# Performance work log

Hardware: AMD Instinct MI355X
Metric: run time of the kernel (lower is better)

Reference implementation:

```python
import jax, jax.numpy as jnp
import numpy as np

SEQ, BATCH, IN_DIM, HID = 2048, 32, 512, 512


def setup_inputs() -> dict:
    key = jax.random.key(0)
    ks = jax.random.split(key, 5)
    scale_ih = 1.0 / np.sqrt(HID)
    return {
        "x": jax.random.normal(ks[0], (SEQ, BATCH, IN_DIM), dtype=jnp.float32),
        "h0": jnp.zeros((BATCH, HID), dtype=jnp.float32),
        "c0": jnp.zeros((BATCH, HID), dtype=jnp.float32),
        "W_ih": jax.random.uniform(ks[1], (4 * HID, IN_DIM), dtype=jnp.float32, minval=-scale_ih, maxval=scale_ih),
        "W_hh": jax.random.uniform(ks[2], (4 * HID, HID), dtype=jnp.float32, minval=-scale_ih, maxval=scale_ih),
        "b_ih": jax.random.uniform(ks[3], (4 * HID,), dtype=jnp.float32, minval=-scale_ih, maxval=scale_ih),
        "b_hh": jax.random.uniform(ks[4], (4 * HID,), dtype=jnp.float32, minval=-scale_ih, maxval=scale_ih),
    }


def reference(x, h0, c0, W_ih, W_hh, b_ih, b_hh):
    # torch.nn.LSTMCell gate order: input, forget, cell(g), output
    b = b_ih + b_hh
    # Precompute input projections for all timesteps: [S, B, 4H]
    x_proj = jnp.einsum("sbi,gi->sbg", x, W_ih) + b

    def step(carry, xp_t):
        h, c = carry
        gates = xp_t + h @ W_hh.T  # [B, 4H]
        i, f, g, o = jnp.split(gates, 4, axis=-1)
        i = jax.nn.sigmoid(i)
        f = jax.nn.sigmoid(f)
        g = jnp.tanh(g)
        o = jax.nn.sigmoid(o)
        c_new = f * c + i * g
        h_new = o * jnp.tanh(c_new)
        return (h_new, c_new), h_new

    (h_T, c_T), hs = jax.lax.scan(step, (h0, c0), x_proj)
    return hs, h_T, c_T
```

## Files before the change

### kernel.cpp

```cpp
#include <hip/hip_runtime.h>
#include <math.h>

#define SEQ    2048
#define BATCH  32
#define IN_DIM 512
#define HID    512
#define GATES  (4*HID)

typedef __attribute__((ext_vector_type(4))) float f32x4;
typedef __attribute__((ext_vector_type(2))) float f32x2;

__device__ inline float fsigmoid(float x) {
    return 1.f / (1.f + __expf(-x));
}
__device__ inline float ftanh(float x) {
    return 1.f - 2.f / (1.f + __expf(2.f * x));
}

__global__ __launch_bounds__(256) void xproj_kernel(
    const float* __restrict__ x,
    const float* __restrict__ Wih,
    const float* __restrict__ bih,
    const float* __restrict__ bhh,
    float* __restrict__ xp,
    int M)
{
    __shared__ float As[16][132];
    __shared__ float Bs[16][132];
    const int tid = threadIdx.x;
    const int nb = blockIdx.x & 15;
    const int mb = blockIdx.x >> 4;
    const int m0 = mb * 128, n0 = nb * 128;
    const int tx = tid & 15, ty = tid >> 4;

    float acc[8][8];
#pragma unroll
    for (int i = 0; i < 8; ++i)
#pragma unroll
        for (int j = 0; j < 8; ++j) acc[i][j] = 0.f;

    for (int kc = 0; kc < 512; kc += 16) {
#pragma unroll
        for (int h = 0; h < 2; ++h) {
            int f4 = tid + 256 * h;
            int r = f4 >> 2, u = f4 & 3;
            float4 va = *(const float4*)(x + (size_t)(m0 + r) * 512 + kc + 4 * u);
            As[4*u+0][r] = va.x; As[4*u+1][r] = va.y;
            As[4*u+2][r] = va.z; As[4*u+3][r] = va.w;
            float4 vb = *(const float4*)(Wih + (size_t)(n0 + r) * 512 + kc + 4 * u);
            Bs[4*u+0][r] = vb.x; Bs[4*u+1][r] = vb.y;
            Bs[4*u+2][r] = vb.z; Bs[4*u+3][r] = vb.w;
        }
        __syncthreads();
#pragma unroll
        for (int kk = 0; kk < 16; ++kk) {
            float4 a0 = *(const float4*)&As[kk][tx * 8];
            float4 a1 = *(const float4*)&As[kk][tx * 8 + 4];
            float4 b0 = *(const float4*)&Bs[kk][ty * 8];
            float4 b1 = *(const float4*)&Bs[kk][ty * 8 + 4];
            float av[8] = {a0.x,a0.y,a0.z,a0.w,a1.x,a1.y,a1.z,a1.w};
            float bv[8] = {b0.x,b0.y,b0.z,b0.w,b1.x,b1.y,b1.z,b1.w};
#pragma unroll
            for (int i = 0; i < 8; ++i)
#pragma unroll
                for (int j = 0; j < 8; ++j) acc[i][j] += av[i] * bv[j];
        }
        __syncthreads();
    }

    float bias[8];
#pragma unroll
    for (int j = 0; j < 8; ++j) {
        int n = n0 + ty * 8 + j;
        bias[j] = bih[n] + bhh[n];
    }
#pragma unroll
    for (int i = 0; i < 8; ++i) {
        size_t base = (size_t)(m0 + tx * 8 + i) * GATES + n0 + ty * 8;
        float4 v0 = make_float4(acc[i][0]+bias[0], acc[i][1]+bias[1],
                                acc[i][2]+bias[2], acc[i][3]+bias[3]);
        float4 v1 = make_float4(acc[i][4]+bias[4], acc[i][5]+bias[5],
                                acc[i][6]+bias[6], acc[i][7]+bias[7]);
        *(float4*)(xp + base)     = v0;
        *(float4*)(xp + base + 4) = v1;
    }
}

__global__ __launch_bounds__(256, 1)
__attribute__((amdgpu_waves_per_eu(1, 1)))
void lstm_coop(
    const float* __restrict__ Whh,
    const float* __restrict__ xp,
    float* __restrict__ hx,
    float* __restrict__ cbuf,
    float* __restrict__ out_hs,
    int t0, int nsteps)
{
    const int w    = blockIdx.x;
    const int g    = w >> 5;
    const int sl   = w & 31;
    const int tid  = threadIdx.x;
    const int hw   = tid >> 6;
    const int lane = tid & 63;
    const int rr   = (lane >> 4) & 3;
    const int kg   = lane & 15;

    __shared__ f32x4 h4[2][512];

    f32x4 wv[32];
#pragma unroll
    for (int gi = 0; gi < 4; ++gi) {
        const float* wr = Whh + (size_t)(512*gi + 16*sl + 4*hw + rr) * 512 + 32*kg;
#pragma unroll
        for (int q = 0; q < 8; ++q) {
            asm volatile("global_load_dwordx4 %0, %1, off"
                         : "=v"(wv[gi*8+q]) : "v"(wr + 4*q));
        }
    }
    asm volatile("s_waitcnt vmcnt(0)" ::: "memory");

    const bool is_tail = ((lane & 12) == 0);
    const int  jb      = lane & 3;
    const int  hid_gl  = 16*sl + 4*hw + rr;
    const int  b_gl    = 4*g + jb;
    const int  slot_p  = 16*(hid_gl & 31) + (hid_gl >> 5);

    float c_reg = 0.f;
    if (is_tail) c_reg = cbuf[(size_t)b_gl * HID + hid_gl];

    for (int t = t0; t < t0 + nsteps; ++t) {
        const int p = t & 1;
        const int xrow = 512*(kg >> 2) + 16*sl + 4*hw + rr;
        const int xb   = 4*g + (kg & 3);
        float xpv = xp[(size_t)(t - t0) * (BATCH * GATES)
                       + (size_t)xb * GATES + xrow];

        const float* rb = hx + ((size_t)p * 8 + g) * 4096;
        const float* p0 = rb + 8 * tid;
        const float* p1 = rb + 8 * tid + 2048;
        const unsigned tu = __float_as_uint((float)t);
        f32x2 a0, a1, a2, a3, b0, b1, b2, b3;
        while (true) {
            asm volatile(
                "global_load_dwordx2 %0, %8, off sc0 sc1\n\t"
                "global_load_dwordx2 %1, %8, off offset:8 sc0 sc1\n\t"
                "global_load_dwordx2 %2, %8, off offset:16 sc0 sc1\n\t"
                "global_load_dwordx2 %3, %8, off offset:24 sc0 sc1\n\t"
                "global_load_dwordx2 %4, %9, off sc0 sc1\n\t"
                "global_load_dwordx2 %5, %9, off offset:8 sc0 sc1\n\t"
                "global_load_dwordx2 %6, %9, off offset:16 sc0 sc1\n\t"
                "global_load_dwordx2 %7, %9, off offset:24 sc0 sc1\n\t"
                "s_waitcnt vmcnt(0)"
                : "=&v"(a0), "=&v"(a1), "=&v"(a2), "=&v"(a3),
                  "=&v"(b0), "=&v"(b1), "=&v"(b2), "=&v"(b3)
                : "v"(p0), "v"(p1)
                : "memory");
            if (__float_as_uint(a0[1]) == tu && __float_as_uint(a1[1]) == tu &&
                __float_as_uint(a2[1]) == tu && __float_as_uint(a3[1]) == tu &&
                __float_as_uint(b0[1]) == tu && __float_as_uint(b1[1]) == tu &&
                __float_as_uint(b2[1]) == tu && __float_as_uint(b3[1]) == tu)
                break;
            __builtin_amdgcn_s_sleep(1);
        }
        {
            f32x4 v0 = {a0[0], a1[0], a2[0], a3[0]};
            f32x4 v1 = {b0[0], b1[0], b2[0], b3[0]};
            h4[p][tid]       = v0;
            h4[p][tid + 256] = v1;
        }
        __syncthreads();

        float acc[16];
#pragma unroll
        for (int m = 0; m < 16; ++m) acc[m] = 0.f;
#pragma unroll
        for (int s = 0; s < 32; ++s) {
            f32x4 hv = h4[p][16*s + kg];
#pragma unroll
            for (int gi = 0; gi < 4; ++gi) {
                float wt = wv[gi*8 + (s >> 2)][s & 3];
                acc[4*gi+0] += wt * hv[0];
                acc[4*gi+1] += wt * hv[1];
                acc[4*gi+2] += wt * hv[2];
                acc[4*gi+3] += wt * hv[3];
            }
        }

        {
            int sel = (kg >> 3) & 1;
#pragma unroll
            for (int m = 0; m < 8; ++m) {
                float mine = sel ? acc[m+8] : acc[m];
                float send = sel ? acc[m]   : acc[m+8];
                acc[m] = mine + __shfl_xor(send, 8, 64);
            }
        }
        {
            int sel = (kg >> 2) & 1;
#pragma unroll
            for (int m = 0; m < 4; ++m) {
                float mine = sel ? acc[m+4] : acc[m];
                float send = sel ? acc[m]   : acc[m+4];
                acc[m] = mine + __shfl_xor(send, 4, 64);
            }
        }
        {
            int sel = (kg >> 1) & 1;
#pragma unroll
            for (int m = 0; m < 2; ++m) {
                float mine = sel ? acc[m+2] : acc[m];
                float send = sel ? acc[m]   : acc[m+2];
                acc[m] = mine + __shfl_xor(send, 2, 64);
            }
        }
        {
            int sel = kg & 1;
            float mine = sel ? acc[1] : acc[0];
            float send = sel ? acc[0] : acc[1];
            acc[0] = mine + __shfl_xor(send, 1, 64);
        }

        float gval = acc[0] + xpv;
        float fv2 = __shfl(gval, (lane & 48) + 4  + jb);
        float gv2 = __shfl(gval, (lane & 48) + 8  + jb);
        float ov2 = __shfl(gval, (lane & 48) + 12 + jb);

        if (is_tail) {
            float iv = fsigmoid(gval);
            float fv = fsigmoid(fv2);
            float gv = ftanh(gv2);
            float ov = fsigmoid(ov2);
            float cn = fv * c_reg + iv * gv;
            float hn = ov * ftanh(cn);
            c_reg = cn;
            f32x2 pkt;
            pkt[0] = hn;
            pkt[1] = (float)(t + 1);
            float* wp = hx + ((size_t)((t + 1) & 1) * 8 + g) * 4096
                        + 8 * slot_p + 2 * jb;
            asm volatile("global_store_dwordx2 %0, %1, off sc0 sc1"
                         :: "v"(wp), "v"(pkt) : "memory");
            out_hs[(size_t)t * (BATCH * HID) + (size_t)b_gl * HID + hid_gl] = hn;
        }
    }

    if (is_tail) cbuf[(size_t)b_gl * HID + hid_gl] = c_reg;
}

__global__ void init_kernel(const float* __restrict__ h0,
                            const float* __restrict__ c0,
                            float* __restrict__ hx,
                            float* __restrict__ cbuf)
{
    int idx = blockIdx.x * 256 + threadIdx.x;
    if (idx < 16384) {
        int g = idx >> 11, G = idx & 2047;
        int slot = G >> 2, c = G & 3;
        int k = 32 * (slot & 15) + (slot >> 4);
        int b = 4 * g + c;
        hx[(size_t)g * 4096 + 2*G]     = h0[(size_t)b * HID + k];
        hx[(size_t)g * 4096 + 2*G + 1] = 0.0f;
        hx[(size_t)32768 + (size_t)g * 4096 + 2*G]     = 0.0f;
        hx[(size_t)32768 + (size_t)g * 4096 + 2*G + 1] = __uint_as_float(0xFFFFFFFFu);
        cbuf[idx] = c0[idx];
    }
}

__global__ void tail_kernel(const float* __restrict__ hx,
                            const float* __restrict__ cbuf,
                            float* __restrict__ out)
{
    int idx = blockIdx.x * 256 + threadIdx.x;
    if (idx < BATCH * HID) {
        int b = idx >> 9, k = idx & 511;
        int g = b >> 2, c = b & 3;
        int slot = 16 * (k & 31) + (k >> 5);
        int G = 4 * slot + c;
        out[(size_t)SEQ * BATCH * HID + idx] = hx[(size_t)g * 4096 + 2*G];
        out[(size_t)SEQ * BATCH * HID + BATCH * HID + idx] = cbuf[idx];
    }
}

extern "C" void kernel_launch(void* const* d_in, const int* in_sizes, int n_in,
                              void* d_out, int out_size, void* d_ws, size_t ws_size,
                              hipStream_t stream)
{
    const float* x   = (const float*)d_in[0];
    const float* h0  = (const float*)d_in[1];
    const float* c0  = (const float*)d_in[2];
    const float* Wih = (const float*)d_in[3];
    const float* Whh = (const float*)d_in[4];
    const float* bih = (const float*)d_in[5];
    const float* bhh = (const float*)d_in[6];
    float* out = (float*)d_out;

    float* hx   = (float*)d_ws;
    float* cbuf = hx + 65536;
    float* xp   = cbuf + 16384;
    size_t used_floats = 65536 + 16384;
    size_t avail = (ws_size / 4 > used_floats) ? (ws_size / 4 - used_floats) : 0;
    int chunk = (int)(avail / (size_t)(BATCH * GATES));
    if (chunk > SEQ) chunk = SEQ;
    chunk &= ~3;
    if (chunk < 4) chunk = 4;

    hipLaunchKernelGGL(init_kernel, dim3(64), dim3(256), 0, stream,
                       h0, c0, hx, cbuf);

    for (int t0 = 0; t0 < SEQ; t0 += chunk) {
        int n = SEQ - t0; if (n > chunk) n = chunk;
        int M = n * BATCH;
        hipLaunchKernelGGL(xproj_kernel, dim3(16 * (M / 128)), dim3(256), 0, stream,
                           x + (size_t)t0 * BATCH * IN_DIM, Wih, bih, bhh, xp, M);

        const float* xp_c = xp;
        int t0_arg = t0, n_arg = n;
        void* args[] = { (void*)&Whh, (void*)&xp_c, (void*)&hx, (void*)&cbuf,
                         (void*)&out, (void*)&t0_arg, (void*)&n_arg };
        hipLaunchCooperativeKernel((void*)lstm_coop, dim3(256), dim3(256),
                                   args, 0, stream);
    }

    hipLaunchKernelGGL(tail_kernel, dim3(64), dim3(256), 0, stream,
                       hx, cbuf, out);
}
```

Measured before the change: 9.368 ms.

## Add fast-path spin with sc1-only loads and prefetch next xproj value

The h-exchange polling loop first spins without sleep using loads scoped only by sc1, which may hit a nearer cache level. After 200 failed polls it falls back to the original sc0 sc1 loads with s_sleep. The producer now writes each packet twice, once with sc1 and once with sc0 sc1, so both cache scopes see the new value. The input-projection load for the next step is issued after polling so its latency overlaps the matvec, at the cost of an extra store per step and possible stale-read retries.

```diff
diff --git a/kernel.cpp b/kernel.cpp
--- a/kernel.cpp
+++ b/kernel.cpp
@@ -128,40 +128,72 @@
     float c_reg = 0.f;
     if (is_tail) c_reg = cbuf[(size_t)b_gl * HID + hid_gl];
 
+    const int xrow = 512*(kg >> 2) + 16*sl + 4*hw + rr;
+    const int xb   = 4*g + (kg & 3);
+    const size_t xoff = (size_t)xb * GATES + xrow;
+
+    float xpv_cur = xp[xoff];
+    bool  fast = true;
+
     for (int t = t0; t < t0 + nsteps; ++t) {
         const int p = t & 1;
-        const int xrow = 512*(kg >> 2) + 16*sl + 4*hw + rr;
-        const int xb   = 4*g + (kg & 3);
-        float xpv = xp[(size_t)(t - t0) * (BATCH * GATES)
-                       + (size_t)xb * GATES + xrow];
 
         const float* rb = hx + ((size_t)p * 8 + g) * 4096;
         const float* p0 = rb + 8 * tid;
         const float* p1 = rb + 8 * tid + 2048;
         const unsigned tu = __float_as_uint((float)t);
         f32x2 a0, a1, a2, a3, b0, b1, b2, b3;
-        while (true) {
-            asm volatile(
-                "global_load_dwordx2 %0, %8, off sc0 sc1\n\t"
-                "global_load_dwordx2 %1, %8, off offset:8 sc0 sc1\n\t"
-                "global_load_dwordx2 %2, %8, off offset:16 sc0 sc1\n\t"
-                "global_load_dwordx2 %3, %8, off offset:24 sc0 sc1\n\t"
-                "global_load_dwordx2 %4, %9, off sc0 sc1\n\t"
-                "global_load_dwordx2 %5, %9, off offset:8 sc0 sc1\n\t"
-                "global_load_dwordx2 %6, %9, off offset:16 sc0 sc1\n\t"
-                "global_load_dwordx2 %7, %9, off offset:24 sc0 sc1\n\t"
-                "s_waitcnt vmcnt(0)"
-                : "=&v"(a0), "=&v"(a1), "=&v"(a2), "=&v"(a3),
-                  "=&v"(b0), "=&v"(b1), "=&v"(b2), "=&v"(b3)
-                : "v"(p0), "v"(p1)
-                : "memory");
-            if (__float_as_uint(a0[1]) == tu && __float_as_uint(a1[1]) == tu &&
-                __float_as_uint(a2[1]) == tu && __float_as_uint(a3[1]) == tu &&
-                __float_as_uint(b0[1]) == tu && __float_as_uint(b1[1]) == tu &&
-                __float_as_uint(b2[1]) == tu && __float_as_uint(b3[1]) == tu)
-                break;
-            __builtin_amdgcn_s_sleep(1);
-        }
+        {
+            int it = 0;
+            while (true) {
+                if (fast) {
+                    asm volatile(
+                        "global_load_dwordx2 %0, %8, off sc1\n\t"
+                        "global_load_dwordx2 %1, %8, off offset:8 sc1\n\t"
+                        "global_load_dwordx2 %2, %8, off offset:16 sc1\n\t"
+                        "global_load_dwordx2 %3, %8, off offset:24 sc1\n\t"
+                        "global_load_dwordx2 %4, %9, off sc1\n\t"
+                        "global_load_dwordx2 %5, %9, off offset:8 sc1\n\t"
+                        "global_load_dwordx2 %6, %9, off offset:16 sc1\n\t"
+                        "global_load_dwordx2 %7, %9, off offset:24 sc1\n\t"
+                        "s_waitcnt vmcnt(0)"
+                        : "=&v"(a0), "=&v"(a1), "=&v"(a2), "=&v"(a3),
+                          "=&v"(b0), "=&v"(b1), "=&v"(b2), "=&v"(b3)
+                        : "v"(p0), "v"(p1)
+                        : "memory");
+                } else {
+                    asm volatile(
+                        "global_load_dwordx2 %0, %8, off sc0 sc1\n\t"
+                        "global_load_dwordx2 %1, %8, off offset:8 sc0 sc1\n\t"
+                        "global_load_dwordx2 %2, %8, off offset:16 sc0 sc1\n\t"
+                        "global_load_dwordx2 %3, %8, off offset:24 sc0 sc1\n\t"
+                        "global_load_dwordx2 %4, %9, off sc0 sc1\n\t"
+                        "global_load_dwordx2 %5, %9, off offset:8 sc0 sc1\n\t"
+                        "global_load_dwordx2 %6, %9, off offset:16 sc0 sc1\n\t"
+                        "global_load_dwordx2 %7, %9, off offset:24 sc0 sc1\n\t"
+                        "s_waitcnt vmcnt(0)"
+                        : "=&v"(a0), "=&v"(a1), "=&v"(a2), "=&v"(a3),
+                          "=&v"(b0), "=&v"(b1), "=&v"(b2), "=&v"(b3)
+                        : "v"(p0), "v"(p1)
+                        : "memory");
+                }
+                if (__float_as_uint(a0[1]) == tu && __float_as_uint(a1[1]) == tu &&
+                    __float_as_uint(a2[1]) == tu && __float_as_uint(a3[1]) == tu &&
+                    __float_as_uint(b0[1]) == tu && __float_as_uint(b1[1]) == tu &&
+                    __float_as_uint(b2[1]) == tu && __float_as_uint(b3[1]) == tu)
+                    break;
+                if (fast) {
+                    if (++it >= 200) fast = false;
+                } else {
+                    __builtin_amdgcn_s_sleep(1);
+                }
+            }
+        }
+
+        float xpv_next = 0.f;
+        if (t + 1 < t0 + nsteps)
+            xpv_next = xp[(size_t)(t + 1 - t0) * (BATCH * GATES) + xoff];
+
         {
             f32x4 v0 = {a0[0], a1[0], a2[0], a3[0]};
             f32x4 v1 = {b0[0], b1[0], b2[0], b3[0]};
@@ -220,7 +252,7 @@
             acc[0] = mine + __shfl_xor(send, 1, 64);
         }
 
-        float gval = acc[0] + xpv;
+        float gval = acc[0] + xpv_cur;
         float fv2 = __shfl(gval, (lane & 48) + 4  + jb);
         float gv2 = __shfl(gval, (lane & 48) + 8  + jb);
         float ov2 = __shfl(gval, (lane & 48) + 12 + jb);
@@ -238,10 +270,13 @@
             pkt[1] = (float)(t + 1);
             float* wp = hx + ((size_t)((t + 1) & 1) * 8 + g) * 4096
                         + 8 * slot_p + 2 * jb;
+            asm volatile("global_store_dwordx2 %0, %1, off sc1"
+                         :: "v"(wp), "v"(pkt) : "memory");
             asm volatile("global_store_dwordx2 %0, %1, off sc0 sc1"
                          :: "v"(wp), "v"(pkt) : "memory");
             out_hs[(size_t)t * (BATCH * HID) + (size_t)b_gl * HID + hid_gl] = hn;
         }
+        xpv_cur = xpv_next;
     }
 
     if (is_tail) cbuf[(size_t)b_gl * HID + hid_gl] = c_reg;
```

New measurement: 11.10 ms. 18.4% more time.
